# Kernel tuning notes

Measured on AMD Instinct MI355X. Metric: run time of the kernel, lower is better.

## Reference

```python
import jax, jax.numpy as jnp
import numpy as np

N = 50000      # nodes
E = 1600000    # message edges (avg degree 32)
EQ = 500000    # link-prediction query edges
IN, HID, OUT, FCH = 128, 128, 64, 256
ALPHA = 0.5


def setup_inputs() -> dict:
    key = jax.random.key(0)
    ks = jax.random.split(key, 8)
    def p(k, shape):
        fan_in = shape[0]
        return jax.random.normal(k, shape, jnp.float32) * (1.0 / np.sqrt(fan_in))
    return {
        "x": jax.random.normal(ks[0], (N, IN), jnp.float32),
        "edge_index": jax.random.randint(ks[1], (2, E), 0, N),
        "edge_label_index": jax.random.randint(ks[2], (2, EQ), 0, N),
        "W1": p(ks[3], (IN, HID)),  "b1": jnp.zeros((HID,), jnp.float32),
        "W2": p(ks[4], (HID, OUT)), "b2": jnp.zeros((OUT,), jnp.float32),
        "Wf1": p(ks[5], (IN, FCH)), "bf1": jnp.zeros((FCH,), jnp.float32),
        "Wf2": p(ks[6], (FCH, OUT)), "bf2": jnp.zeros((OUT,), jnp.float32),
    }


def reference(x, edge_index, edge_label_index, W1, b1, W2, b2, Wf1, bf1, Wf2, bf2):
    n = x.shape[0]
    # GCN self-loops + symmetric normalization (PyG GCNConv defaults)
    loop = jnp.arange(n)
    src = jnp.concatenate([edge_index[0], loop])
    dst = jnp.concatenate([edge_index[1], loop])
    deg = jax.ops.segment_sum(jnp.ones_like(dst, jnp.float32), dst, num_segments=n)
    dinv = jnp.where(deg > 0, jax.lax.rsqrt(deg), 0.0)
    norm = dinv[src] * dinv[dst]  # [E+N]

    def gcn(h, W, b):
        h = h @ W                                  # transform first (PyG order)
        msg = norm[:, None] * h[src]               # gather + scale per edge
        return jax.ops.segment_sum(msg, dst, num_segments=n) + b

    x_gcn = jax.nn.relu(gcn(x, W1, b1))
    x_gcn = gcn(x_gcn, W2, b2)
    x_fc = jax.nn.relu(x @ Wf1 + bf1) @ Wf2 + bf2
    z = x_gcn * (1.0 - ALPHA) + x_fc * ALPHA       # [N, OUT]
    # edge dot-product decode
    return jnp.sum(z[edge_label_index[0]] * z[edge_label_index[1]], axis=1)
```

## Files before the change

### kernel.cpp

```cpp
#include <hip/hip_runtime.h>

#define FIN   128
#define FHID  128
#define FOUT  64
#define FFC   256
#define CHUNK 4096
#define BKBITS 7
#define BKN   128
#define ECAP  4608

typedef __attribute__((ext_vector_type(8))) short          bf16x8;
typedef __attribute__((ext_vector_type(4))) float          f32x4;
typedef __attribute__((ext_vector_type(2))) float          f32x2;
typedef __attribute__((ext_vector_type(8))) unsigned short u16x8;

static __device__ __forceinline__ unsigned short f2bf(float f) {
    unsigned int u = __float_as_uint(f);
    u = (u + 0x7fffu + ((u >> 16) & 1u)) >> 16;
    return (unsigned short)u;
}
static __device__ __forceinline__ float bf2f(unsigned short s) {
    return __uint_as_float(((unsigned int)s) << 16);
}
static __device__ __forceinline__ void accum_fp8(float* acc, uint4 g) {
    f32x2 p;
    p = __builtin_amdgcn_cvt_pk_f32_fp8(g.x, false); acc[0]  += p.x; acc[1]  += p.y;
    p = __builtin_amdgcn_cvt_pk_f32_fp8(g.x, true);  acc[2]  += p.x; acc[3]  += p.y;
    p = __builtin_amdgcn_cvt_pk_f32_fp8(g.y, false); acc[4]  += p.x; acc[5]  += p.y;
    p = __builtin_amdgcn_cvt_pk_f32_fp8(g.y, true);  acc[6]  += p.x; acc[7]  += p.y;
    p = __builtin_amdgcn_cvt_pk_f32_fp8(g.z, false); acc[8]  += p.x; acc[9]  += p.y;
    p = __builtin_amdgcn_cvt_pk_f32_fp8(g.z, true);  acc[10] += p.x; acc[11] += p.y;
    p = __builtin_amdgcn_cvt_pk_f32_fp8(g.w, false); acc[12] += p.x; acc[13] += p.y;
    p = __builtin_amdgcn_cvt_pk_f32_fp8(g.w, true);  acc[14] += p.x; acc[15] += p.y;
}

__global__ __launch_bounds__(256) void binA_kernel(
    const int* __restrict__ src, const int* __restrict__ dst,
    int* __restrict__ bcur, unsigned int* __restrict__ ebuf, int E)
{
    __shared__ int hist[512];
    __shared__ int rstart[512];
    __shared__ int lcur[512];
    int t = threadIdx.x;
    hist[t] = 0; hist[t + 256] = 0; lcur[t] = 0; lcur[t + 256] = 0;
    __syncthreads();
    int e0 = blockIdx.x * CHUNK;
    int e1 = min(e0 + CHUNK, E);
    for (int e = e0 + t; e < e1; e += 256)
        atomicAdd(&hist[dst[e] >> BKBITS], 1);
    __syncthreads();
    if (hist[t])       rstart[t]       = atomicAdd(&bcur[t],       hist[t]);
    if (hist[t + 256]) rstart[t + 256] = atomicAdd(&bcur[t + 256], hist[t + 256]);
    __syncthreads();
    for (int e = e0 + t; e < e1; e += 256) {
        int s = src[e], d = dst[e];
        int b = d >> BKBITS;
        int pos = rstart[b] + atomicAdd(&lcur[b], 1);
        if (pos < ECAP)
            ebuf[(size_t)b * ECAP + pos] =
                ((unsigned)s << BKBITS) | ((unsigned)d & (BKN - 1));
    }
}

__global__ __launch_bounds__(256) void binB_kernel(
    const unsigned int* __restrict__ ebuf, const int* __restrict__ bcnt,
    int2* __restrict__ rp2, int* __restrict__ col, float* __restrict__ dinv,
    const float* __restrict__ x, unsigned char* __restrict__ xs,
    int N)
{
    __shared__ int cnt[128];
    __shared__ int tmp[256];
    __shared__ int ccur[128];
    __shared__ int scur[256];
    __shared__ float sdinv[128];
    __shared__ unsigned int skey[ECAP];
    int b = blockIdx.x;
    int t = threadIdx.x;
    size_t base = (size_t)b * ECAP;
    int ne = min(bcnt[b], ECAP);
    if (t < 128) cnt[t] = 0;
    scur[t] = 0;
    __syncthreads();
    for (int e = t; e < ne; e += 256) {
        unsigned int k = ebuf[base + e];
        atomicAdd(&cnt[k & (BKN - 1)], 1);
        atomicAdd(&scur[k >> 15], 1);
    }
    __syncthreads();
    int c = (t < 128) ? cnt[t] : 0;
    tmp[t] = c;
    __syncthreads();
    int acc = c;
    for (int off = 1; off < 128; off <<= 1) {
        int a = (t >= off) ? tmp[t - off] : 0;
        __syncthreads();
        acc += a; tmp[t] = acc;
        __syncthreads();
    }
    if (t < 128) {
        float di = rsqrtf((float)c + 1.0f);
        sdinv[t] = di;
        int node = b * BKN + t;
        int st = (int)base + acc - c;
        if (node < N) { dinv[node] = di; rp2[node] = make_int2(st, st + c); }
        ccur[t] = st;
    }
    __syncthreads();
    int sv = scur[t];
    tmp[t] = sv;
    __syncthreads();
    int sacc = sv;
    for (int off = 1; off < 256; off <<= 1) {
        int a = (t >= off) ? tmp[t - off] : 0;
        __syncthreads();
        sacc += a; tmp[t] = sacc;
        __syncthreads();
    }
    scur[t] = sacc - sv;
    __syncthreads();
    for (int e = t; e < ne; e += 256) {
        unsigned int k = ebuf[base + e];
        int pos = atomicAdd(&scur[k >> 15], 1);
        skey[pos] = k;
    }
    __syncthreads();
    for (int w = 0; w < ne; w += 256) {
        int e = w + t;
        if (e < ne) {
            unsigned int k = skey[e];
            int pos = atomicAdd(&ccur[k & (BKN - 1)], 1);
            col[pos] = (int)(k >> BKBITS);
        }
        __syncthreads();
    }
    int nl0 = t >> 3;
    int f0 = (t & 7) << 4;
    #pragma unroll
    for (int it = 0; it < 4; it++) {
        int nl = it * 32 + nl0;
        int gn = b * BKN + nl;
        if (gn >= N) continue;
        float d2 = sdinv[nl];
        const float* xr = x + (size_t)gn * FIN + f0;
        float4 va = *(const float4*)(xr);
        float4 vb = *(const float4*)(xr + 4);
        float4 vc = *(const float4*)(xr + 8);
        float4 vd = *(const float4*)(xr + 12);
        float f[16] = { va.x * d2, va.y * d2, va.z * d2, va.w * d2,
                        vb.x * d2, vb.y * d2, vb.z * d2, vb.w * d2,
                        vc.x * d2, vc.y * d2, vc.z * d2, vc.w * d2,
                        vd.x * d2, vd.y * d2, vd.z * d2, vd.w * d2 };
        uint4 w;
        w.x = 0; w.y = 0; w.z = 0; w.w = 0;
        w.x = __builtin_amdgcn_cvt_pk_fp8_f32(f[0],  f[1],  w.x, false);
        w.x = __builtin_amdgcn_cvt_pk_fp8_f32(f[2],  f[3],  w.x, true);
        w.y = __builtin_amdgcn_cvt_pk_fp8_f32(f[4],  f[5],  w.y, false);
        w.y = __builtin_amdgcn_cvt_pk_fp8_f32(f[6],  f[7],  w.y, true);
        w.z = __builtin_amdgcn_cvt_pk_fp8_f32(f[8],  f[9],  w.z, false);
        w.z = __builtin_amdgcn_cvt_pk_fp8_f32(f[10], f[11], w.z, true);
        w.w = __builtin_amdgcn_cvt_pk_fp8_f32(f[12], f[13], w.w, false);
        w.w = __builtin_amdgcn_cvt_pk_fp8_f32(f[14], f[15], w.w, true);
        *(uint4*)(xs + (size_t)gn * 128 + f0) = w;
    }
}

__global__ __launch_bounds__(256) void fc_fused_kernel(
    const float* __restrict__ X,
    const float* __restrict__ Wf1,
    const float* __restrict__ Wf2,
    const float* __restrict__ bias1, const float* __restrict__ bias2,
    float* __restrict__ C, int M)
{
    __shared__ __align__(16) unsigned short lds[32768];
    const int tid  = threadIdx.x;
    const int lane = tid & 63;
    const int wave = tid >> 6;
    const int m = lane & 15;
    const int q = lane >> 4;
    const int rowbase = blockIdx.x * 64 + wave * 16;
    const int row = rowbase + m;

    for (int i = tid; i < 4096; i += 256) {
        int sl = i >> 8, n = i & 255;
        u16x8 o;
        #pragma unroll
        for (int j = 0; j < 8; j++) o[j] = f2bf(Wf1[(sl * 8 + j) * 256 + n]);
        ((u16x8*)lds)[(n << 4) | (sl ^ (n & 7))] = o;
    }
    __syncthreads();

    f32x4 acc[16] = {};
    const float* arow = X + (size_t)row * FIN + q * 8;
    for (int k0 = 0; k0 < 128; k0 += 32) {
        bf16x8 a = {};
        if (row < M) {
            float4 a0 = *(const float4*)(arow + k0);
            float4 a1 = *(const float4*)(arow + k0 + 4);
            a[0] = (short)f2bf(a0.x); a[1] = (short)f2bf(a0.y);
            a[2] = (short)f2bf(a0.z); a[3] = (short)f2bf(a0.w);
            a[4] = (short)f2bf(a1.x); a[5] = (short)f2bf(a1.y);
            a[6] = (short)f2bf(a1.z); a[7] = (short)f2bf(a1.w);
        }
        int sl = q + (k0 >> 3);
        #pragma unroll
        for (int c = 0; c < 16; c++) {
            int cc = c * 16 + m;
            bf16x8 b = ((const bf16x8*)lds)[(cc << 4) | (sl ^ (cc & 7))];
            acc[c] = __builtin_amdgcn_mfma_f32_16x16x32_bf16(a, b, acc[c], 0, 0, 0);
        }
    }
    __syncthreads();

    for (int i = tid; i < 2048; i += 256) {
        int sl = i >> 6, n = i & 63;
        u16x8 o;
        #pragma unroll
        for (int j = 0; j < 8; j++) o[j] = f2bf(Wf2[(sl * 8 + j) * 64 + n]);
        ((u16x8*)lds)[2048 + ((n << 5) | (sl ^ (n & 7)))] = o;
    }
    #pragma unroll
    for (int c = 0; c < 16; c++) {
        int cc = c * 16 + m;
        float bv = bias1[cc];
        #pragma unroll
        for (int r = 0; r < 4; r++) {
            int rr = wave * 16 + q * 4 + r;
            float v = fmaxf(acc[c][r] + bv, 0.f);
            lds[rr * 256 + ((((cc >> 3) ^ (rr & 7)) << 3) | (cc & 7))] = f2bf(v);
        }
    }
    __syncthreads();

    f32x4 acc2[4] = {};
    {
        int rr = wave * 16 + m;
        for (int k0 = 0; k0 < 256; k0 += 32) {
            int sl = q + (k0 >> 3);
            bf16x8 a = ((const bf16x8*)lds)[(rr << 5) | (sl ^ (rr & 7))];
            #pragma unroll
            for (int c = 0; c < 4; c++) {
                int cc = c * 16 + m;
                bf16x8 b = ((const bf16x8*)lds)[2048 + ((cc << 5) | (sl ^ (cc & 7)))];
                acc2[c] = __builtin_amdgcn_mfma_f32_16x16x32_bf16(a, b, acc2[c], 0, 0, 0);
            }
        }
    }
    __syncthreads();

    constexpr int ROWB = 4 * 16 * 4 + 16;
    unsigned char* wbase = (unsigned char*)lds + wave * 16 * ROWB;
    #pragma unroll
    for (int c = 0; c < 4; c++) {
        int lc = c * 16 + m;
        float bv = bias2[lc];
        #pragma unroll
        for (int r = 0; r < 4; r++)
            ((float*)(wbase + (q * 4 + r) * ROWB))[lc] = acc2[c][r] + bv;
    }
    #pragma unroll
    for (int p = 0; p < 4; p++) {
        int r2 = p * 4 + (lane >> 4);
        int bo = (lane & 15) * 16;
        int gr = rowbase + r2;
        if (gr < M) {
            uint4 v = *(const uint4*)(wbase + r2 * ROWB + bo);
            *(uint4*)((unsigned char*)C + (size_t)gr * FOUT * 4 + bo) = v;
        }
    }
}

__global__ __launch_bounds__(256) void gcn_fused_kernel(
    const unsigned char* __restrict__ xs, const int2* __restrict__ rp2,
    const int* __restrict__ col, const float* __restrict__ dinv,
    const float* __restrict__ W1,
    const float* __restrict__ W2,
    const float* __restrict__ bias1,
    unsigned short* __restrict__ C, int M)
{
    __shared__ __align__(16) unsigned short lds[32768];
    const int tid  = threadIdx.x;
    const int lane = tid & 63;
    const int wave = tid >> 6;
    const int m = lane & 15;
    const int q = lane >> 4;
    const int rowbase = blockIdx.x * 64 + wave * 16;

    for (int i = tid; i < 2048; i += 256) {
        int sl = i >> 7, n = i & 127;
        u16x8 o;
        #pragma unroll
        for (int j = 0; j < 8; j++) o[j] = f2bf(W1[(sl * 8 + j) * 128 + n]);
        ((u16x8*)lds)[1024 + ((n << 4) | (sl ^ (n & 7)))] = o;
    }
    for (int i = tid; i < 1024; i += 256) {
        int sl = i >> 6, n = i & 63;
        u16x8 o;
        #pragma unroll
        for (int j = 0; j < 8; j++) o[j] = f2bf(W2[(sl * 8 + j) * 64 + n]);
        ((u16x8*)lds)[3072 + ((n << 4) | (sl ^ (n & 7)))] = o;
    }

    {
        int nls = tid >> 3;
        int f0 = (tid & 7) << 4;
        int c80 = (tid & 7) * 2;
        const unsigned char* gbase = xs + f0;
        #pragma unroll
        for (int pass = 0; pass < 2; pass++) {
            int lnl = pass * 32 + nls;
            int node = blockIdx.x * 64 + lnl;
            u16x8 o0 = {}, o1 = {};
            if (node < M) {
                float acc[16] = {};
                accum_fp8(acc, *(const uint4*)(gbase + (size_t)node * 128));
                int2 se = rp2[node];
                int e = se.x, end = se.y;
                for (; e + 4 <= end; e += 4) {
                    int s0 = col[e], s1 = col[e + 1];
                    int s2 = col[e + 2], s3 = col[e + 3];
                    uint4 g0 = *(const uint4*)(gbase + (size_t)s0 * 128);
                    uint4 g1 = *(const uint4*)(gbase + (size_t)s1 * 128);
                    uint4 g2 = *(const uint4*)(gbase + (size_t)s2 * 128);
                    uint4 g3 = *(const uint4*)(gbase + (size_t)s3 * 128);
                    accum_fp8(acc, g0); accum_fp8(acc, g1);
                    accum_fp8(acc, g2); accum_fp8(acc, g3);
                }
                for (; e < end; e++)
                    accum_fp8(acc, *(const uint4*)(gbase + (size_t)col[e] * 128));
                float di = dinv[node];
                #pragma unroll
                for (int j = 0; j < 8; j++) {
                    o0[j] = f2bf(di * acc[j]);
                    o1[j] = f2bf(di * acc[8 + j]);
                }
            }
            ((u16x8*)lds)[lnl * 16 + (c80 ^ (lnl & 7))]       = o0;
            ((u16x8*)lds)[lnl * 16 + ((c80 + 1) ^ (lnl & 7))] = o1;
        }
    }
    __syncthreads();

    f32x4 acc[8] = {};
    for (int k0 = 0; k0 < 128; k0 += 32) {
        int sl = q + (k0 >> 3);
        int lr = wave * 16 + m;
        bf16x8 a = ((const bf16x8*)lds)[lr * 16 + (sl ^ (lr & 7))];
        #pragma unroll
        for (int c = 0; c < 8; c++) {
            int cc = c * 16 + m;
            bf16x8 b = ((const bf16x8*)lds)[1024 + ((cc << 4) | (sl ^ (cc & 7)))];
            acc[c] = __builtin_amdgcn_mfma_f32_16x16x32_bf16(a, b, acc[c], 0, 0, 0);
        }
    }
    __syncthreads();

    #pragma unroll
    for (int c = 0; c < 8; c++) {
        int cc = c * 16 + m;
        float bv = bias1[cc];
        #pragma unroll
        for (int r = 0; r < 4; r++) {
            int rr = wave * 16 + q * 4 + r;
            float v = fmaxf(acc[c][r] + bv, 0.f);
            lds[8192 + rr * 128 + ((((cc >> 3) ^ (rr & 7)) << 3) | (cc & 7))] = f2bf(v);
        }
    }
    __syncthreads();

    f32x4 acc2[4] = {};
    {
        int rr = wave * 16 + m;
        for (int k0 = 0; k0 < 128; k0 += 32) {
            int sl = q + (k0 >> 3);
            bf16x8 a = ((const bf16x8*)lds)[1024 + ((rr << 4) | (sl ^ (rr & 7)))];
            #pragma unroll
            for (int c = 0; c < 4; c++) {
                int cc = c * 16 + m;
                bf16x8 b = ((const bf16x8*)lds)[3072 + ((cc << 4) | (sl ^ (cc & 7)))];
                acc2[c] = __builtin_amdgcn_mfma_f32_16x16x32_bf16(a, b, acc2[c], 0, 0, 0);
            }
        }
    }
    float rs[4];
    #pragma unroll
    for (int r = 0; r < 4; r++) {
        int gr = rowbase + q * 4 + r;
        rs[r] = (gr < M) ? dinv[gr] : 1.0f;
    }
    __syncthreads();

    constexpr int ROWB = 4 * 16 * 2 + 16;
    unsigned char* wbase = (unsigned char*)lds + wave * 16 * ROWB;
    #pragma unroll
    for (int c = 0; c < 4; c++) {
        int lc = c * 16 + m;
        #pragma unroll
        for (int r = 0; r < 4; r++)
            ((unsigned short*)(wbase + (q * 4 + r) * ROWB))[lc] =
                f2bf(acc2[c][r] * rs[r]);
    }
    #pragma unroll
    for (int p = 0; p < 2; p++) {
        int r2 = p * 8 + (lane >> 3);
        int bo = (lane & 7) * 16;
        int gr = rowbase + r2;
        if (gr < M) {
            uint4 v = *(const uint4*)(wbase + r2 * ROWB + bo);
            *(uint4*)((unsigned char*)C + (size_t)gr * FOUT * 2 + bo) = v;
        }
    }
}

__global__ __launch_bounds__(256) void pull2_kernel(
    const unsigned short* __restrict__ t2s, const int2* __restrict__ rp2,
    const int* __restrict__ col, const float* __restrict__ dinv,
    const float* __restrict__ xfc, const float* __restrict__ b2,
    unsigned short* __restrict__ zbf, int N)
{
    int tid = threadIdx.x;
    int node = blockIdx.x * 32 + (tid >> 3);
    if (node >= N) return;
    int f0 = (tid & 7) << 3;
    const unsigned short* base = t2s + f0;
    u16x8 own = *(const u16x8*)(base + (size_t)node * FOUT);
    float acc[8];
    #pragma unroll
    for (int j = 0; j < 8; j++) acc[j] = bf2f(own[j]);
    int2 se = rp2[node];
    int e = se.x, end = se.y;
    for (; e + 4 <= end; e += 4) {
        int s0 = col[e], s1 = col[e + 1], s2 = col[e + 2], s3 = col[e + 3];
        u16x8 v0 = *(const u16x8*)(base + (size_t)s0 * FOUT);
        u16x8 v1 = *(const u16x8*)(base + (size_t)s1 * FOUT);
        u16x8 v2 = *(const u16x8*)(base + (size_t)s2 * FOUT);
        u16x8 v3 = *(const u16x8*)(base + (size_t)s3 * FOUT);
        #pragma unroll
        for (int j = 0; j < 8; j++)
            acc[j] += (bf2f(v0[j]) + bf2f(v1[j])) + (bf2f(v2[j]) + bf2f(v3[j]));
    }
    for (; e < end; e++) {
        u16x8 v = *(const u16x8*)(base + (size_t)col[e] * FOUT);
        #pragma unroll
        for (int j = 0; j < 8; j++) acc[j] += bf2f(v[j]);
    }
    float di = dinv[node];
    float4 x0 = *(const float4*)(xfc + (size_t)node * FOUT + f0);
    float4 x1 = *(const float4*)(xfc + (size_t)node * FOUT + f0 + 4);
    float4 bb0 = *(const float4*)(b2 + f0);
    float4 bb1 = *(const float4*)(b2 + f0 + 4);
    float xf[8] = { x0.x, x0.y, x0.z, x0.w, x1.x, x1.y, x1.z, x1.w };
    float bv[8] = { bb0.x, bb0.y, bb0.z, bb0.w, bb1.x, bb1.y, bb1.z, bb1.w };
    u16x8 o;
    #pragma unroll
    for (int j = 0; j < 8; j++)
        o[j] = f2bf(0.5f * (di * acc[j] + bv[j]) + 0.5f * xf[j]);
    *(u16x8*)(zbf + (size_t)node * FOUT + f0) = o;
}

__global__ void decode_kernel(
    const unsigned short* __restrict__ zbf, const int* __restrict__ eli,
    float* __restrict__ out, int Q)
{
    int tid = blockIdx.x * blockDim.x + threadIdx.x;
    int q = tid >> 3;
    if (q >= Q) return;
    int lane = tid & 7;
    int a = eli[q];
    int b = eli[Q + q];
    u16x8 va = *(const u16x8*)(zbf + (size_t)a * FOUT + lane * 8);
    u16x8 vb = *(const u16x8*)(zbf + (size_t)b * FOUT + lane * 8);
    float s = 0.f;
    #pragma unroll
    for (int j = 0; j < 8; j++) s += bf2f(va[j]) * bf2f(vb[j]);
    s += __shfl_down(s, 4, 8);
    s += __shfl_down(s, 2, 8);
    s += __shfl_down(s, 1, 8);
    if (lane == 0) out[q] = s;
}

extern "C" void kernel_launch(void* const* d_in, const int* in_sizes, int n_in,
                              void* d_out, int out_size, void* d_ws, size_t ws_size,
                              hipStream_t stream)
{
    const float* x   = (const float*)d_in[0];
    const int*   ei  = (const int*)  d_in[1];
    const int*   eli = (const int*)  d_in[2];
    const float* W1  = (const float*)d_in[3];
    const float* b1  = (const float*)d_in[4];
    const float* W2  = (const float*)d_in[5];
    const float* b2  = (const float*)d_in[6];
    const float* Wf1 = (const float*)d_in[7];
    const float* bf1 = (const float*)d_in[8];
    const float* Wf2 = (const float*)d_in[9];
    const float* bf2 = (const float*)d_in[10];
    float* out = (float*)d_out;

    const int N = in_sizes[0] / FIN;
    const int E = in_sizes[1] / 2;
    const int Q = in_sizes[2] / 2;
    const int* src = ei;
    const int* dst = ei + E;
    const int NBK = (N + BKN - 1) >> BKBITS;
    const int NBA = (E + CHUNK - 1) / CHUNK;

    char* p = (char*)d_ws;
    float* dinv = (float*)p;             p += (size_t)N * 4;
    int2*  rp2  = (int2*)p;              p += (size_t)N * 8;
    int*   bcur = (int*)p;               p += 2048;
    float* xfc = (float*)p;              p += (size_t)N * FOUT * 4;
    unsigned char* xs = (unsigned char*)p;     p += (size_t)N * 128;
    unsigned int* ebuf = (unsigned int*)p;  p += (size_t)NBK * ECAP * 4;
    int*   col  = (int*)p;               p += (size_t)NBK * ECAP * 4;
    unsigned short* t2s  = (unsigned short*)p; p += (size_t)N * FOUT * 2;
    unsigned short* zbf  = (unsigned short*)p; p += (size_t)N * FOUT * 2;

    const int TB = 256;

    hipMemsetAsync(bcur, 0, 2048, stream);

    fc_fused_kernel<<<(N + 63) / 64, TB, 0, stream>>>(
        x, Wf1, Wf2, bf1, bf2, xfc, N);

    binA_kernel<<<NBA, TB, 0, stream>>>(src, dst, bcur, ebuf, E);

    binB_kernel<<<NBK, TB, 0, stream>>>(ebuf, bcur, rp2, col, dinv, x, xs, N);

    gcn_fused_kernel<<<(N + 63) / 64, TB, 0, stream>>>(
        xs, rp2, col, dinv, W1, W2, b1, t2s, N);

    pull2_kernel<<<(N + 31) / 32, TB, 0, stream>>>(
        t2s, rp2, col, dinv, xfc, b2, zbf, N);

    {
        long total = (long)Q * 8;
        decode_kernel<<<(int)((total + TB - 1) / TB), TB, 0, stream>>>(
            zbf, eli, out, Q);
    }
}
```

Before: 272.5 us.

## Split fused GCN layer into separate gather kernel and MFMA GEMM kernel

The fused kernel that gathered neighbour features and then ran both MFMA GEMMs is split in two. A new pull1 kernel does the fp8 neighbour aggregation into a bf16 global buffer, and gcn_kernel reads that buffer straight from global memory for the first GEMM. This aims to decouple the latency-bound gather from the heavy-LDS GEMM: the smaller LDS footprint and one node per 8 threads should raise occupancy and gather parallelism. The cost is an extra launch plus a round trip of an N×128 bf16 intermediate through global memory.

```diff
diff --git a/kernel.cpp b/kernel.cpp
--- a/kernel.cpp
+++ b/kernel.cpp
@@ -269,86 +269,85 @@
     }
 }
 
-__global__ __launch_bounds__(256) void gcn_fused_kernel(
+__global__ __launch_bounds__(256) void pull1_kernel(
     const unsigned char* __restrict__ xs, const int2* __restrict__ rp2,
     const int* __restrict__ col, const float* __restrict__ dinv,
+    unsigned short* __restrict__ aggx, int N)
+{
+    int tid = threadIdx.x;
+    int node = blockIdx.x * 32 + (tid >> 3);
+    if (node >= N) return;
+    int f0 = (tid & 7) << 4;
+    const unsigned char* base = xs + f0;
+    float acc[16] = {};
+    accum_fp8(acc, *(const uint4*)(base + (size_t)node * 128));
+    int2 se = rp2[node];
+    int e = se.x, end = se.y;
+    for (; e + 4 <= end; e += 4) {
+        int s0 = col[e], s1 = col[e + 1], s2 = col[e + 2], s3 = col[e + 3];
+        uint4 g0 = *(const uint4*)(base + (size_t)s0 * 128);
+        uint4 g1 = *(const uint4*)(base + (size_t)s1 * 128);
+        uint4 g2 = *(const uint4*)(base + (size_t)s2 * 128);
+        uint4 g3 = *(const uint4*)(base + (size_t)s3 * 128);
+        accum_fp8(acc, g0); accum_fp8(acc, g1);
+        accum_fp8(acc, g2); accum_fp8(acc, g3);
+    }
+    for (; e < end; e++)
+        accum_fp8(acc, *(const uint4*)(base + (size_t)col[e] * 128));
+    float di = dinv[node];
+    u16x8 o0, o1;
+    #pragma unroll
+    for (int j = 0; j < 8; j++) {
+        o0[j] = f2bf(di * acc[j]);
+        o1[j] = f2bf(di * acc[8 + j]);
+    }
+    *(u16x8*)(aggx + (size_t)node * FIN + f0)     = o0;
+    *(u16x8*)(aggx + (size_t)node * FIN + f0 + 8) = o1;
+}
+
+__global__ __launch_bounds__(256) void gcn_kernel(
+    const unsigned short* __restrict__ A,
     const float* __restrict__ W1,
     const float* __restrict__ W2,
     const float* __restrict__ bias1,
+    const float* __restrict__ rowscale,
     unsigned short* __restrict__ C, int M)
 {
-    __shared__ __align__(16) unsigned short lds[32768];
+    __shared__ __align__(16) unsigned short lds[24576];
     const int tid  = threadIdx.x;
     const int lane = tid & 63;
     const int wave = tid >> 6;
     const int m = lane & 15;
     const int q = lane >> 4;
     const int rowbase = blockIdx.x * 64 + wave * 16;
+    const int row = rowbase + m;
 
     for (int i = tid; i < 2048; i += 256) {
         int sl = i >> 7, n = i & 127;
         u16x8 o;
         #pragma unroll
         for (int j = 0; j < 8; j++) o[j] = f2bf(W1[(sl * 8 + j) * 128 + n]);
-        ((u16x8*)lds)[1024 + ((n << 4) | (sl ^ (n & 7)))] = o;
+        ((u16x8*)lds)[(n << 4) | (sl ^ (n & 7))] = o;
     }
     for (int i = tid; i < 1024; i += 256) {
         int sl = i >> 6, n = i & 63;
         u16x8 o;
         #pragma unroll
         for (int j = 0; j < 8; j++) o[j] = f2bf(W2[(sl * 8 + j) * 64 + n]);
-        ((u16x8*)lds)[3072 + ((n << 4) | (sl ^ (n & 7)))] = o;
-    }
-
-    {
-        int nls = tid >> 3;
-        int f0 = (tid & 7) << 4;
-        int c80 = (tid & 7) * 2;
-        const unsigned char* gbase = xs + f0;
-        #pragma unroll
-        for (int pass = 0; pass < 2; pass++) {
-            int lnl = pass * 32 + nls;
-            int node = blockIdx.x * 64 + lnl;
-            u16x8 o0 = {}, o1 = {};
-            if (node < M) {
-                float acc[16] = {};
-                accum_fp8(acc, *(const uint4*)(gbase + (size_t)node * 128));
-                int2 se = rp2[node];
-                int e = se.x, end = se.y;
-                for (; e + 4 <= end; e += 4) {
-                    int s0 = col[e], s1 = col[e + 1];
-                    int s2 = col[e + 2], s3 = col[e + 3];
-                    uint4 g0 = *(const uint4*)(gbase + (size_t)s0 * 128);
-                    uint4 g1 = *(const uint4*)(gbase + (size_t)s1 * 128);
-                    uint4 g2 = *(const uint4*)(gbase + (size_t)s2 * 128);
-                    uint4 g3 = *(const uint4*)(gbase + (size_t)s3 * 128);
-                    accum_fp8(acc, g0); accum_fp8(acc, g1);
-                    accum_fp8(acc, g2); accum_fp8(acc, g3);
-                }
-                for (; e < end; e++)
-                    accum_fp8(acc, *(const uint4*)(gbase + (size_t)col[e] * 128));
-                float di = dinv[node];
-                #pragma unroll
-                for (int j = 0; j < 8; j++) {
-                    o0[j] = f2bf(di * acc[j]);
-                    o1[j] = f2bf(di * acc[8 + j]);
-                }
-            }
-            ((u16x8*)lds)[lnl * 16 + (c80 ^ (lnl & 7))]       = o0;
-            ((u16x8*)lds)[lnl * 16 + ((c80 + 1) ^ (lnl & 7))] = o1;
-        }
+        ((u16x8*)lds)[2048 + ((n << 4) | (sl ^ (n & 7)))] = o;
     }
     __syncthreads();
 
     f32x4 acc[8] = {};
+    const unsigned short* arow = A + (size_t)row * FIN + q * 8;
     for (int k0 = 0; k0 < 128; k0 += 32) {
+        bf16x8 a = {};
+        if (row < M) a = *(const bf16x8*)(arow + k0);
         int sl = q + (k0 >> 3);
-        int lr = wave * 16 + m;
-        bf16x8 a = ((const bf16x8*)lds)[lr * 16 + (sl ^ (lr & 7))];
         #pragma unroll
         for (int c = 0; c < 8; c++) {
             int cc = c * 16 + m;
-            bf16x8 b = ((const bf16x8*)lds)[1024 + ((cc << 4) | (sl ^ (cc & 7)))];
+            bf16x8 b = ((const bf16x8*)lds)[(cc << 4) | (sl ^ (cc & 7))];
             acc[c] = __builtin_amdgcn_mfma_f32_16x16x32_bf16(a, b, acc[c], 0, 0, 0);
         }
     }
@@ -362,7 +361,7 @@
         for (int r = 0; r < 4; r++) {
             int rr = wave * 16 + q * 4 + r;
             float v = fmaxf(acc[c][r] + bv, 0.f);
-            lds[8192 + rr * 128 + ((((cc >> 3) ^ (rr & 7)) << 3) | (cc & 7))] = f2bf(v);
+            lds[rr * 128 + ((((cc >> 3) ^ (rr & 7)) << 3) | (cc & 7))] = f2bf(v);
         }
     }
     __syncthreads();
@@ -372,11 +371,11 @@
         int rr = wave * 16 + m;
         for (int k0 = 0; k0 < 128; k0 += 32) {
             int sl = q + (k0 >> 3);
-            bf16x8 a = ((const bf16x8*)lds)[1024 + ((rr << 4) | (sl ^ (rr & 7)))];
+            bf16x8 a = ((const bf16x8*)lds)[(rr << 4) | (sl ^ (rr & 7))];
             #pragma unroll
             for (int c = 0; c < 4; c++) {
                 int cc = c * 16 + m;
-                bf16x8 b = ((const bf16x8*)lds)[3072 + ((cc << 4) | (sl ^ (cc & 7)))];
+                bf16x8 b = ((const bf16x8*)lds)[2048 + ((cc << 4) | (sl ^ (cc & 7)))];
                 acc2[c] = __builtin_amdgcn_mfma_f32_16x16x32_bf16(a, b, acc2[c], 0, 0, 0);
             }
         }
@@ -385,7 +384,7 @@
     #pragma unroll
     for (int r = 0; r < 4; r++) {
         int gr = rowbase + q * 4 + r;
-        rs[r] = (gr < M) ? dinv[gr] : 1.0f;
+        rs[r] = (gr < M) ? rowscale[gr] : 1.0f;
     }
     __syncthreads();
 
@@ -511,6 +510,7 @@
     unsigned char* xs = (unsigned char*)p;     p += (size_t)N * 128;
     unsigned int* ebuf = (unsigned int*)p;  p += (size_t)NBK * ECAP * 4;
     int*   col  = (int*)p;               p += (size_t)NBK * ECAP * 4;
+    unsigned short* aggx = (unsigned short*)p; p += (size_t)N * FIN * 2;
     unsigned short* t2s  = (unsigned short*)p; p += (size_t)N * FOUT * 2;
     unsigned short* zbf  = (unsigned short*)p; p += (size_t)N * FOUT * 2;
 
@@ -525,8 +525,10 @@
 
     binB_kernel<<<NBK, TB, 0, stream>>>(ebuf, bcur, rp2, col, dinv, x, xs, N);
 
-    gcn_fused_kernel<<<(N + 63) / 64, TB, 0, stream>>>(
-        xs, rp2, col, dinv, W1, W2, b1, t2s, N);
+    pull1_kernel<<<(N + 31) / 32, TB, 0, stream>>>(xs, rp2, col, dinv, aggx, N);
+
+    gcn_kernel<<<(N + 63) / 64, TB, 0, stream>>>(
+        aggx, W1, W2, b1, dinv, t2s, N);
 
     pull2_kernel<<<(N + 31) / 32, TB, 0, stream>>>(
         t2s, rp2, col, dinv, xfc, b2, zbf, N);
```

Measured after the change: 260.3 us. 1.05x faster.
